# Optimization experiments

Measured on AMD Instinct MI355X. Metric: run time of the kernel, lower is better.

Reference implementation:

```python
import jax, jax.numpy as jnp
import numpy as np

B, T = 64, 512
VOCAB, E, H = 20, 64, 128
D = 2 * H            # 256, bidirectional LSTM output dim
NH, KD = 8, D // 8   # 8 heads, key_dim 32
DU, OUT = 256, 128
NEG = -1e9


def _lstm_scan(x, mask, W, U, b):
    # x: [B,T,E], mask: [B,T] bool. Keras gate order: i, f, g(c), o.
    Bb = x.shape[0]
    Hh = U.shape[0]
    def step(carry, inp):
        h, c = carry
        xt, mt = inp                      # [B,E], [B]
        z = xt @ W + h @ U + b            # [B,4H]
        i, f, g, o = jnp.split(z, 4, axis=-1)
        c_new = jax.nn.sigmoid(f) * c + jax.nn.sigmoid(i) * jnp.tanh(g)
        h_new = jax.nn.sigmoid(o) * jnp.tanh(c_new)
        m = mt[:, None]
        h = jnp.where(m, h_new, h)        # freeze state/output on masked steps
        c = jnp.where(m, c_new, c)
        return (h, c), h
    h0 = jnp.zeros((Bb, Hh), x.dtype)
    _, ys = jax.lax.scan(step, (h0, h0), (jnp.swapaxes(x, 0, 1), mask.T))
    return jnp.swapaxes(ys, 0, 1)         # [B,T,H]


def setup_inputs() -> dict:
    key = jax.random.key(0)
    ks = jax.random.split(key, 24)
    g = lambda k, shape, s: (jax.random.normal(k, shape, jnp.float32) * s)
    inp = {
        'sequences': jax.random.randint(ks[0], (B, T), 0, VOCAB),
        'emb': g(ks[1], (VOCAB, E), 0.05),
        # forward LSTM
        'Wf': g(ks[2], (E, 4 * H), 0.05), 'Uf': g(ks[3], (H, 4 * H), 0.05), 'bf': jnp.zeros((4 * H,), jnp.float32),
        # backward LSTM
        'Wb': g(ks[4], (E, 4 * H), 0.05), 'Ub': g(ks[5], (H, 4 * H), 0.05), 'bb': jnp.zeros((4 * H,), jnp.float32),
        # MHA projections
        'Wq': g(ks[6], (D, NH, KD), 0.05), 'bq': jnp.zeros((NH, KD), jnp.float32),
        'Wk': g(ks[7], (D, NH, KD), 0.05), 'bk': jnp.zeros((NH, KD), jnp.float32),
        'Wv': g(ks[8], (D, NH, KD), 0.05), 'bv': jnp.zeros((NH, KD), jnp.float32),
        'Wo': g(ks[9], (NH, KD, D), 0.05), 'bo': jnp.zeros((D,), jnp.float32),
        # MLP head (input is concat of avg+max pool -> 2*D)
        'W1': g(ks[10], (2 * D, DU), 0.05), 'b1': jnp.zeros((DU,), jnp.float32),
        'W2': g(ks[11], (DU, DU // 2), 0.05), 'b2': jnp.zeros((DU // 2,), jnp.float32),
        'W3': g(ks[12], (DU // 2, OUT), 0.05), 'b3': jnp.zeros((OUT,), jnp.float32),
    }
    return inp


def _forward(sequences, emb, Wf, Uf, bf, Wb, Ub, bb, Wq, bq, Wk, bk, Wv, bv, Wo, bo, W1, b1, W2, b2, W3, b3):
    mask = sequences != 0                       # mask_zero=True
    x = emb[sequences]                          # [B,T,E]
    fwd = _lstm_scan(x, mask, Wf, Uf, bf)
    bwd = _lstm_scan(x[:, ::-1], mask[:, ::-1], Wb, Ub, bb)[:, ::-1]
    h = jnp.concatenate([fwd, bwd], axis=-1)    # [B,T,D]
    # Multi-head self-attention (key-masked, Keras MHA math)
    q = jnp.einsum('btd,dhk->bthk', h, Wq) + bq
    k = jnp.einsum('btd,dhk->bthk', h, Wk) + bk
    v = jnp.einsum('btd,dhk->bthk', h, Wv) + bv
    scores = jnp.einsum('bthk,bshk->bhts', q, k) / jnp.sqrt(jnp.float32(KD))
    scores = jnp.where(mask[:, None, None, :], scores, NEG)
    attn = jax.nn.softmax(scores, axis=-1)      # [B,H,T,T]
    ctx = jnp.einsum('bhts,bshk->bthk', attn, v)
    att = jnp.einsum('bthk,hkd->btd', ctx, Wo) + bo   # [B,T,D]
    # dual pooling (masked mean + masked max)
    mf = mask[..., None].astype(att.dtype)
    avg = (att * mf).sum(axis=1) / jnp.maximum(mf.sum(axis=1), 1.0)
    mx = jnp.where(mask[..., None], att, NEG).max(axis=1)
    p = jnp.concatenate([avg, mx], axis=-1)     # [B,2D]
    x1 = jax.nn.relu(p @ W1 + b1)
    x2 = jax.nn.relu(x1 @ W2 + b2)
    return x2 @ W3 + b3                         # [B,OUT]


def reference(sequences, emb, Wf, Uf, bf, Wb, Ub, bb, Wq, bq, Wk, bk, Wv, bv, Wo, bo, W1, b1, W2, b2, W3, b3):
    return _forward(sequences, emb, Wf, Uf, bf, Wb, Ub, bb, Wq, bq, Wk, bk, Wv, bv, Wo, bo, W1, b1, W2, b2, W3, b3)
```

## Files before the change

### kernel.cpp

```cpp
#include <hip/hip_runtime.h>
#include <math.h>

#define B_ 64
#define T_ 512
#define E_ 64
#define H_ 128
#define NH_ 8
#define KD_ 32
#define BT_ (B_ * T_)
#define NEG_ -1e9f

typedef __attribute__((ext_vector_type(8))) short bf16x8_t;
typedef __attribute__((ext_vector_type(4))) float f32x4_t;
typedef __attribute__((ext_vector_type(2))) float f32x2_t;
typedef unsigned short ushort_t;
typedef unsigned int uint_t;

__device__ __forceinline__ float sigmoidf_(float x) {
    return 1.f / (1.f + __expf(-x));
}
__device__ __forceinline__ float tanhf_(float x) {
    return 1.f - 2.f / (1.f + __expf(2.f * x));
}

__device__ __forceinline__ ushort_t bf16_rne(float x) {
    uint_t u = __float_as_uint(x);
    uint_t r = (u + 0x7FFFu + ((u >> 16) & 1u)) >> 16;
    return (ushort_t)r;
}
__device__ __forceinline__ float bf16_to_f(ushort_t h) {
    return __uint_as_float(((uint_t)h) << 16);
}
__device__ __forceinline__ void split_bf16(float x, ushort_t& h, ushort_t& l) {
    h = bf16_rne(x);
    l = bf16_rne(x - bf16_to_f(h));
}

__device__ __forceinline__ float qswap1(float x) {
    return __int_as_float(__builtin_amdgcn_mov_dpp(__float_as_int(x), 0xB1, 0xF, 0xF, true));
}
__device__ __forceinline__ float qswap2(float x) {
    return __int_as_float(__builtin_amdgcn_mov_dpp(__float_as_int(x), 0x4E, 0xF, 0xF, true));
}

__global__ void prep_kernel(
    const float* __restrict__ emb,
    const float* __restrict__ Wf, const float* __restrict__ bf,
    const float* __restrict__ Wb, const float* __restrict__ bb,
    const float* __restrict__ Wq, const float* __restrict__ Wk,
    const float* __restrict__ Wv, const float* __restrict__ Wo,
    ushort_t* __restrict__ Wqh, ushort_t* __restrict__ Wql,
    ushort_t* __restrict__ Wkh, ushort_t* __restrict__ Wkl,
    ushort_t* __restrict__ Wvh, ushort_t* __restrict__ Wvl,
    ushort_t* __restrict__ Woh, ushort_t* __restrict__ Wol,
    float* __restrict__ embWf, float* __restrict__ embWb)
{
    const int blk = blockIdx.x, tid = threadIdx.x;
    if (blk < 1024) {
        const int m = blk >> 8, k = blk & 255;
        const float* W = (m == 0) ? Wq : (m == 1) ? Wk : (m == 2) ? Wv : Wo;
        ushort_t* Bh = (m == 0) ? Wqh : (m == 1) ? Wkh : (m == 2) ? Wvh : Woh;
        ushort_t* Bl = (m == 0) ? Wql : (m == 1) ? Wkl : (m == 2) ? Wvl : Wol;
        float v = W[k * 256 + tid];
        ushort_t h, l;
        split_bf16(v, h, l);
        Bh[tid * 256 + k] = h;
        Bl[tid * 256 + k] = l;
    } else {
        const int e = blk - 1024;
        const int dir = e >> 1, half = e & 1;
        const float* W = dir ? Wb : Wf;
        const float* bias = dir ? bb : bf;
        float* dst = dir ? embWb : embWf;
        const int np = half * 256 + tid;
        const int gin = ((np & 3) << 7) + (np >> 2);
        for (int v = 0; v < 20; ++v) {
            float acc = bias[gin];
            for (int k = 0; k < 64; ++k)
                acc = fmaf(emb[v * 64 + k], W[k * 512 + gin], acc);
            dst[v * 512 + np] = acc;
        }
    }
}

__global__ __launch_bounds__(256, 2) void gemm_mfma3(
    const ushort_t* __restrict__ Ah, const ushort_t* __restrict__ Al,
    const ushort_t* __restrict__ Bh, const ushort_t* __restrict__ Bl,
    const float* __restrict__ bias, float* __restrict__ C,
    int M, int N)
{
    __shared__ __align__(16) ushort_t Alds[2][128 * 40];
    __shared__ __align__(16) ushort_t Blds[2][128 * 40];

    const int tid = threadIdx.x;
    const int ntn = N >> 7;
    const int bm = blockIdx.x / ntn, bn = blockIdx.x % ntn;
    const int m0 = bm << 7, n0 = bn << 7;

    const int w = tid >> 6;
    const int wr = w >> 1, wc = w & 1;
    const int lane = tid & 63;
    const int fr = lane & 15, kg = lane >> 4;

    const int sr = tid >> 1;
    const int sh = (tid & 1) << 4;

    f32x4_t acc[4][4];
#pragma unroll
    for (int i = 0; i < 4; ++i)
#pragma unroll
        for (int j = 0; j < 4; ++j) acc[i][j] = (f32x4_t){0.f, 0.f, 0.f, 0.f};

    for (int ks = 0; ks < 8; ++ks) {
        const int k0 = ks << 5;
        __syncthreads();
        {
            const size_t ga = (size_t)(m0 + sr) * 256 + k0 + sh;
            const size_t gb = (size_t)(n0 + sr) * 256 + k0 + sh;
            const int ld = sr * 40 + sh;
            const uint4* pah = (const uint4*)(Ah + ga);
            const uint4* pal = (const uint4*)(Al + ga);
            const uint4* pbh = (const uint4*)(Bh + gb);
            const uint4* pbl = (const uint4*)(Bl + gb);
            uint4* qah = (uint4*)&Alds[0][ld];
            uint4* qal = (uint4*)&Alds[1][ld];
            uint4* qbh = (uint4*)&Blds[0][ld];
            uint4* qbl = (uint4*)&Blds[1][ld];
            qah[0] = pah[0]; qah[1] = pah[1];
            qal[0] = pal[0]; qal[1] = pal[1];
            qbh[0] = pbh[0]; qbh[1] = pbh[1];
            qbl[0] = pbl[0]; qbl[1] = pbl[1];
        }
        __syncthreads();

        bf16x8_t ah[4], al[4], bh[4], bl[4];
#pragma unroll
        for (int i = 0; i < 4; ++i) {
            const int ra = (wr * 64 + i * 16 + fr) * 40 + kg * 8;
            const int rb = (wc * 64 + i * 16 + fr) * 40 + kg * 8;
            ah[i] = *(const bf16x8_t*)&Alds[0][ra];
            al[i] = *(const bf16x8_t*)&Alds[1][ra];
            bh[i] = *(const bf16x8_t*)&Blds[0][rb];
            bl[i] = *(const bf16x8_t*)&Blds[1][rb];
        }
#pragma unroll
        for (int i = 0; i < 4; ++i)
#pragma unroll
            for (int j = 0; j < 4; ++j) {
                acc[i][j] = __builtin_amdgcn_mfma_f32_16x16x32_bf16(
                    ah[i], bh[j], acc[i][j], 0, 0, 0);
                acc[i][j] = __builtin_amdgcn_mfma_f32_16x16x32_bf16(
                    ah[i], bl[j], acc[i][j], 0, 0, 0);
                acc[i][j] = __builtin_amdgcn_mfma_f32_16x16x32_bf16(
                    al[i], bh[j], acc[i][j], 0, 0, 0);
            }
    }

#pragma unroll
    for (int j = 0; j < 4; ++j) {
        const int col = n0 + wc * 64 + j * 16 + fr;
        const float bv = bias[col];
#pragma unroll
        for (int i = 0; i < 4; ++i) {
#pragma unroll
            for (int r = 0; r < 4; ++r) {
                const int row = m0 + wr * 64 + i * 16 + kg * 4 + r;
                C[(size_t)row * N + col] = acc[i][j][r] + bv;
            }
        }
    }
}

__global__ __launch_bounds__(512, 1) void lstm_scan(
    const int* __restrict__ seq,
    const float* __restrict__ embWf, const float* __restrict__ embWb,
    const float* __restrict__ Uf, const float* __restrict__ Ub,
    ushort_t* __restrict__ hch, ushort_t* __restrict__ hcl)
{
    const int w = blockIdx.x;
    const int dir = w & 1, b = w >> 1;
    const float* eW = dir ? embWb : embWf;
    const float* U  = dir ? Ub  : Uf;
    const int tid = threadIdx.x;
    const int jj = tid >> 2, ks = tid & 3;

    __shared__ __align__(16) float hbuf[2][4][36];
    __shared__ int tkl[T_];

    f32x2_t u2[4][16];
#pragma unroll
    for (int g = 0; g < 4; ++g)
#pragma unroll
        for (int kk = 0; kk < 16; ++kk) {
            const int kb_ = 32 * ks + 2 * kk;
            u2[g][kk] = (f32x2_t){
                U[(size_t)kb_ * 512 + g * 128 + jj],
                U[(size_t)(kb_ + 1) * 512 + g * 128 + jj] };
        }

    tkl[tid] = seq[b * T_ + tid];
    if (tid < 2 * 4 * 36) ((float*)hbuf)[tid] = 0.f;

    float h_cur = 0.f, c_cur = 0.f;
    ushort_t* hoh = hch + (size_t)b * T_ * 256 + dir * 128;
    ushort_t* hol = hcl + (size_t)b * T_ * 256 + dir * 128;

    __syncthreads();

    int te = dir ? (T_ - 1) : 0;
    int tok = tkl[te];
    float4 xwv = *(const float4*)&eW[tok * 512 + jj * 4];

    int p = 0;
    for (int t = 0; t < T_; ++t) {
        const int te_n  = dir ? (te - 1) : (te + 1);
        const int te_pf = (t == T_ - 1) ? te : te_n;
        const int tok_n = tkl[te_pf];
        const float4 xw_n = *(const float4*)&eW[tok_n * 512 + jj * 4];

        f32x2_t ac0 = {0.f, 0.f}, ac1 = {0.f, 0.f};
        f32x2_t ac2 = {0.f, 0.f}, ac3 = {0.f, 0.f};
        const f32x2_t* hc2 = (const f32x2_t*)hbuf[p][ks];
#pragma unroll
        for (int c = 0; c < 16; ++c) {
            const f32x2_t h2 = hc2[c];
            ac0 = __builtin_elementwise_fma(h2, u2[0][c], ac0);
            ac1 = __builtin_elementwise_fma(h2, u2[1][c], ac1);
            ac2 = __builtin_elementwise_fma(h2, u2[2][c], ac2);
            ac3 = __builtin_elementwise_fma(h2, u2[3][c], ac3);
        }
        float a0 = ac0.x + ac0.y, a1 = ac1.x + ac1.y;
        float a2 = ac2.x + ac2.y, a3 = ac3.x + ac3.y;
        a0 += qswap1(a0); a0 += qswap2(a0);
        a1 += qswap1(a1); a1 += qswap2(a1);
        a2 += qswap1(a2); a2 += qswap2(a2);
        a3 += qswap1(a3); a3 += qswap2(a3);

        const float zi = xwv.x + a0, zf = xwv.y + a1;
        const float zg = xwv.z + a2, zo = xwv.w + a3;
        const float cn = fmaf(sigmoidf_(zf), c_cur, sigmoidf_(zi) * tanhf_(zg));
        const float hn = sigmoidf_(zo) * tanhf_(cn);
        const bool mt = (tok != 0);
        const float hm = mt ? hn : h_cur;
        c_cur = mt ? cn : c_cur;
        h_cur = hm;

        if ((jj >> 5) == ks) hbuf[1 - p][ks][jj & 31] = hm;
        if (ks == 0) {
            ushort_t hh, hl;
            split_bf16(hm, hh, hl);
            hoh[(size_t)te * 256 + jj] = hh;
            hol[(size_t)te * 256 + jj] = hl;
        }
        __syncthreads();
        p ^= 1; te = te_n; tok = tok_n; xwv = xw_n;
    }
}

__global__ __launch_bounds__(256, 2) void attn_fused(
    const int* __restrict__ seq,
    const float* __restrict__ q, const float* __restrict__ kk,
    const float* __restrict__ vv,
    ushort_t* __restrict__ cxh, ushort_t* __restrict__ cxl)
{
    const int wg = blockIdx.x;
    const int b = wg >> 3, h = wg & 7;
    const int tid = threadIdx.x;

    __shared__ __align__(16) float Ks[16][32];
    __shared__ __align__(16) float Vs[16][32];
    __shared__ float mk[16];

    float qA[32], qB[32];
    {
        const float* qp  = q + (((size_t)(b * T_) + tid) * NH_ + h) * KD_;
        const float* qp2 = qp + (size_t)256 * NH_ * KD_;
#pragma unroll
        for (int k = 0; k < 32; k += 4) {
            float4 v0 = *(const float4*)(qp + k);
            float4 v1 = *(const float4*)(qp2 + k);
            qA[k] = v0.x; qA[k + 1] = v0.y; qA[k + 2] = v0.z; qA[k + 3] = v0.w;
            qB[k] = v1.x; qB[k + 1] = v1.y; qB[k + 2] = v1.z; qB[k + 3] = v1.w;
        }
    }
    float ctxA[32], ctxB[32];
#pragma unroll
    for (int k = 0; k < 32; ++k) { ctxA[k] = 0.f; ctxB[k] = 0.f; }
    float mA = -1e30f, mB = -1e30f, lA = 0.f, lB = 0.f;

    const int lr = (tid & 127) >> 3;
    const int lc = (tid & 7) << 2;
    const bool loadV = (tid >= 128);

    for (int c = 0; c < T_ / 16; ++c) {
        const int s0 = c << 4;
        __syncthreads();
        {
            const float* src = (loadV ? vv : kk) +
                (((size_t)(b * T_) + s0 + lr) * NH_ + h) * KD_ + lc;
            float4 v = *(const float4*)src;
            if (loadV) *(float4*)&Vs[lr][lc] = v;
            else       *(float4*)&Ks[lr][lc] = v;
            if (tid < 16) mk[tid] = (seq[b * T_ + s0 + tid] != 0) ? 0.f : 1.f;
        }
        __syncthreads();

        float sA[16], sB[16];
#pragma unroll
        for (int s = 0; s < 16; ++s) {
            float dA = 0.f, dB = 0.f;
#pragma unroll
            for (int k = 0; k < 32; k += 4) {
                float4 k4 = *(const float4*)&Ks[s][k];
                dA = fmaf(k4.x, qA[k], dA); dA = fmaf(k4.y, qA[k + 1], dA);
                dA = fmaf(k4.z, qA[k + 2], dA); dA = fmaf(k4.w, qA[k + 3], dA);
                dB = fmaf(k4.x, qB[k], dB); dB = fmaf(k4.y, qB[k + 1], dB);
                dB = fmaf(k4.z, qB[k + 2], dB); dB = fmaf(k4.w, qB[k + 3], dB);
            }
            const float SCL = 0.17677669529663687f;
            const bool masked = (mk[s] > 0.5f);
            sA[s] = masked ? NEG_ : dA * SCL;
            sB[s] = masked ? NEG_ : dB * SCL;
        }
        float cmA = sA[0], cmB = sB[0];
#pragma unroll
        for (int s = 1; s < 16; ++s) {
            cmA = fmaxf(cmA, sA[s]); cmB = fmaxf(cmB, sB[s]);
        }
        const float mnA = fmaxf(mA, cmA), mnB = fmaxf(mB, cmB);
        const float alA = __expf(mA - mnA), alB = __expf(mB - mnB);
        float psA = 0.f, psB = 0.f;
#pragma unroll
        for (int s = 0; s < 16; ++s) {
            float pa = __expf(sA[s] - mnA); sA[s] = pa; psA += pa;
            float pb = __expf(sB[s] - mnB); sB[s] = pb; psB += pb;
        }
        lA = fmaf(lA, alA, psA); lB = fmaf(lB, alB, psB);
        mA = mnA; mB = mnB;
#pragma unroll
        for (int k = 0; k < 32; ++k) { ctxA[k] *= alA; ctxB[k] *= alB; }
#pragma unroll
        for (int s = 0; s < 16; ++s) {
#pragma unroll
            for (int k = 0; k < 32; k += 4) {
                float4 v4 = *(const float4*)&Vs[s][k];
                ctxA[k]     = fmaf(sA[s], v4.x, ctxA[k]);
                ctxA[k + 1] = fmaf(sA[s], v4.y, ctxA[k + 1]);
                ctxA[k + 2] = fmaf(sA[s], v4.z, ctxA[k + 2]);
                ctxA[k + 3] = fmaf(sA[s], v4.w, ctxA[k + 3]);
                ctxB[k]     = fmaf(sB[s], v4.x, ctxB[k]);
                ctxB[k + 1] = fmaf(sB[s], v4.y, ctxB[k + 1]);
                ctxB[k + 2] = fmaf(sB[s], v4.z, ctxB[k + 2]);
                ctxB[k + 3] = fmaf(sB[s], v4.w, ctxB[k + 3]);
            }
        }
    }

    const float iA = 1.f / lA, iB = 1.f / lB;
    ushort_t* chA = cxh + (((size_t)(b * T_) + tid) * NH_ + h) * KD_;
    ushort_t* clA = cxl + (((size_t)(b * T_) + tid) * NH_ + h) * KD_;
    ushort_t* chB = chA + (size_t)256 * NH_ * KD_;
    ushort_t* clB = clA + (size_t)256 * NH_ * KD_;
#pragma unroll
    for (int k = 0; k < 32; ++k) {
        ushort_t hA, lA_, hB, lB_;
        split_bf16(ctxA[k] * iA, hA, lA_);
        split_bf16(ctxB[k] * iB, hB, lB_);
        chA[k] = hA; clA[k] = lA_;
        chB[k] = hB; clB[k] = lB_;
    }
}

__global__ __launch_bounds__(256) void poolmlp_kernel(
    const int* __restrict__ seq, const float* __restrict__ att,
    const float* __restrict__ W1, const float* __restrict__ b1,
    const float* __restrict__ W2, const float* __restrict__ b2,
    const float* __restrict__ W3, const float* __restrict__ b3,
    float* __restrict__ out)
{
    const int b = blockIdx.x;
    const int tid = threadIdx.x;
    __shared__ float mk[T_];
    __shared__ float pl[512];
    __shared__ float x1l[256];
    __shared__ float x2l[128];

    for (int t = tid; t < T_; t += 256)
        mk[t] = (seq[b * T_ + t] != 0) ? 1.f : 0.f;
    __syncthreads();

    float sum = 0.f, mx = NEG_, cnt = 0.f;
    for (int t = 0; t < T_; ++t) {
        const float a = att[((size_t)b * T_ + t) * 256 + tid];
        const float m = mk[t];
        cnt += m;
        sum = fmaf(m, a, sum);
        mx = fmaxf(mx, (m > 0.5f) ? a : NEG_);
    }
    pl[tid] = sum / fmaxf(cnt, 1.f);
    pl[256 + tid] = mx;
    __syncthreads();

    {
        float acc = b1[tid];
        for (int k = 0; k < 512; ++k) acc = fmaf(pl[k], W1[k * 256 + tid], acc);
        x1l[tid] = fmaxf(acc, 0.f);
    }
    __syncthreads();
    if (tid < 128) {
        float acc = b2[tid];
        for (int k = 0; k < 256; ++k) acc = fmaf(x1l[k], W2[k * 128 + tid], acc);
        x2l[tid] = fmaxf(acc, 0.f);
    }
    __syncthreads();
    if (tid < 128) {
        float acc = b3[tid];
        for (int k = 0; k < 128; ++k) acc = fmaf(x2l[k], W3[k * 128 + tid], acc);
        out[b * 128 + tid] = acc;
    }
}

extern "C" void kernel_launch(void* const* d_in, const int* in_sizes, int n_in,
                              void* d_out, int out_size, void* d_ws, size_t ws_size,
                              hipStream_t stream)
{
    (void)in_sizes; (void)n_in; (void)out_size; (void)ws_size;
    const int*   seq = (const int*)d_in[0];
    const float* emb = (const float*)d_in[1];
    const float* Wf  = (const float*)d_in[2];
    const float* Uf  = (const float*)d_in[3];
    const float* bf  = (const float*)d_in[4];
    const float* Wb  = (const float*)d_in[5];
    const float* Ub  = (const float*)d_in[6];
    const float* bb  = (const float*)d_in[7];
    const float* Wq  = (const float*)d_in[8];
    const float* bq  = (const float*)d_in[9];
    const float* Wk  = (const float*)d_in[10];
    const float* bk  = (const float*)d_in[11];
    const float* Wv  = (const float*)d_in[12];
    const float* bv  = (const float*)d_in[13];
    const float* Wo  = (const float*)d_in[14];
    const float* bo  = (const float*)d_in[15];
    const float* W1  = (const float*)d_in[16];
    const float* b1  = (const float*)d_in[17];
    const float* W2  = (const float*)d_in[18];
    const float* b2  = (const float*)d_in[19];
    const float* W3  = (const float*)d_in[20];
    const float* b3  = (const float*)d_in[21];
    float* out = (float*)d_out;
    float* ws  = (float*)d_ws;

    float* qb   = ws;
    float* kb   = ws + 8388608;
    float* vb   = ws + 16777216;
    ushort_t* cxh = (ushort_t*)(ws + 25165824);
    ushort_t* cxl = cxh + (size_t)BT_ * 256;
    ushort_t* hch = (ushort_t*)(ws + 33554432);
    ushort_t* hcl = hch + (size_t)BT_ * 256;
    float* attb = ws + 33554432;
    ushort_t* wt = (ushort_t*)(ws + 41943040);
    ushort_t* Wqh = wt + 0 * 65536, *Wql = wt + 1 * 65536;
    ushort_t* Wkh = wt + 2 * 65536, *Wkl = wt + 3 * 65536;
    ushort_t* Wvh = wt + 4 * 65536, *Wvl = wt + 5 * 65536;
    ushort_t* Woh = wt + 6 * 65536, *Wol = wt + 7 * 65536;
    float* embWf = ws + 41943040 + 262144;
    float* embWb = embWf + 20 * 512;

    const dim3 blk256(256), blk512(512);

    prep_kernel<<<dim3(1028), blk256, 0, stream>>>(
        emb, Wf, bf, Wb, bb, Wq, Wk, Wv, Wo,
        Wqh, Wql, Wkh, Wkl, Wvh, Wvl, Woh, Wol, embWf, embWb);

    lstm_scan<<<dim3(128), blk512, 0, stream>>>(
        seq, embWf, embWb, Uf, Ub, hch, hcl);

    gemm_mfma3<<<dim3((BT_ / 128) * 2), blk256, 0, stream>>>(
        hch, hcl, Wqh, Wql, bq, qb, BT_, 256);
    gemm_mfma3<<<dim3((BT_ / 128) * 2), blk256, 0, stream>>>(
        hch, hcl, Wkh, Wkl, bk, kb, BT_, 256);
    gemm_mfma3<<<dim3((BT_ / 128) * 2), blk256, 0, stream>>>(
        hch, hcl, Wvh, Wvl, bv, vb, BT_, 256);

    attn_fused<<<dim3(B_ * NH_), blk256, 0, stream>>>(seq, qb, kb, vb, cxh, cxl);

    gemm_mfma3<<<dim3((BT_ / 128) * 2), blk256, 0, stream>>>(
        cxh, cxl, Woh, Wol, bo, attb, BT_, 256);

    poolmlp_kernel<<<dim3(B_), blk256, 0, stream>>>(
        seq, attb, W1, b1, W2, b2, W3, b3, out);
}
```

Before: 945.2 us.

## Fuse QKV projections into one GEMM and slim LSTM scan block

The three Q/K/V projection GEMMs become a single N=768 GEMM with concatenated weights and bias, and attention reads Q, K and V from the interleaved buffer. This removes two launches and re-reads of the hidden-state input. The LSTM scan now uses 256 threads with a 2-way k-split instead of 4-way, so each step needs one DPP reduction instead of two. It keeps the embedding-times-W table in LDS and replaces __syncthreads with a raw waitcnt+barrier. In exchange, each LSTM thread holds twice as many U registers (256 floats), which risks spills and a longer serial FMA chain per step.

Result: slower. 1.057 ms (+11.8%).

```diff
diff --git a/kernel.cpp b/kernel.cpp
--- a/kernel.cpp
+++ b/kernel.cpp
@@ -39,9 +39,6 @@
 __device__ __forceinline__ float qswap1(float x) {
     return __int_as_float(__builtin_amdgcn_mov_dpp(__float_as_int(x), 0xB1, 0xF, 0xF, true));
 }
-__device__ __forceinline__ float qswap2(float x) {
-    return __int_as_float(__builtin_amdgcn_mov_dpp(__float_as_int(x), 0x4E, 0xF, 0xF, true));
-}
 
 __global__ void prep_kernel(
     const float* __restrict__ emb,
@@ -49,24 +46,28 @@
     const float* __restrict__ Wb, const float* __restrict__ bb,
     const float* __restrict__ Wq, const float* __restrict__ Wk,
     const float* __restrict__ Wv, const float* __restrict__ Wo,
-    ushort_t* __restrict__ Wqh, ushort_t* __restrict__ Wql,
-    ushort_t* __restrict__ Wkh, ushort_t* __restrict__ Wkl,
-    ushort_t* __restrict__ Wvh, ushort_t* __restrict__ Wvl,
-    ushort_t* __restrict__ Woh, ushort_t* __restrict__ Wol,
-    float* __restrict__ embWf, float* __restrict__ embWb)
+    const float* __restrict__ bq, const float* __restrict__ bk,
+    const float* __restrict__ bv,
+    ushort_t* __restrict__ wqkvh, ushort_t* __restrict__ wqkvl,
+    ushort_t* __restrict__ woh, ushort_t* __restrict__ wol,
+    float* __restrict__ embWf, float* __restrict__ embWb,
+    float* __restrict__ qkvb)
 {
     const int blk = blockIdx.x, tid = threadIdx.x;
     if (blk < 1024) {
         const int m = blk >> 8, k = blk & 255;
         const float* W = (m == 0) ? Wq : (m == 1) ? Wk : (m == 2) ? Wv : Wo;
-        ushort_t* Bh = (m == 0) ? Wqh : (m == 1) ? Wkh : (m == 2) ? Wvh : Woh;
-        ushort_t* Bl = (m == 0) ? Wql : (m == 1) ? Wkl : (m == 2) ? Wvl : Wol;
         float v = W[k * 256 + tid];
         ushort_t h, l;
         split_bf16(v, h, l);
-        Bh[tid * 256 + k] = h;
-        Bl[tid * 256 + k] = l;
-    } else {
+        if (m < 3) {
+            wqkvh[(m * 256 + tid) * 256 + k] = h;
+            wqkvl[(m * 256 + tid) * 256 + k] = l;
+        } else {
+            woh[tid * 256 + k] = h;
+            wol[tid * 256 + k] = l;
+        }
+    } else if (blk < 1028) {
         const int e = blk - 1024;
         const int dir = e >> 1, half = e & 1;
         const float* W = dir ? Wb : Wf;
@@ -80,6 +81,10 @@
                 acc = fmaf(emb[v * 64 + k], W[k * 512 + gin], acc);
             dst[v * 512 + np] = acc;
         }
+    } else {
+        qkvb[tid] = bq[tid];
+        qkvb[256 + tid] = bk[tid];
+        qkvb[512 + tid] = bv[tid];
     }
 }
 
@@ -171,7 +176,7 @@
     }
 }
 
-__global__ __launch_bounds__(512, 1) void lstm_scan(
+__global__ __launch_bounds__(256, 1) void lstm_scan(
     const int* __restrict__ seq,
     const float* __restrict__ embWf, const float* __restrict__ embWb,
     const float* __restrict__ Uf, const float* __restrict__ Ub,
@@ -182,24 +187,31 @@
     const float* eW = dir ? embWb : embWf;
     const float* U  = dir ? Ub  : Uf;
     const int tid = threadIdx.x;
-    const int jj = tid >> 2, ks = tid & 3;
-
-    __shared__ __align__(16) float hbuf[2][4][36];
+    const int jj = tid >> 1, ks = tid & 1;
+
+    __shared__ __align__(16) float eWl[20 * 512];
+    __shared__ __align__(16) float hbuf[2][136];
     __shared__ int tkl[T_];
 
-    f32x2_t u2[4][16];
+    f32x2_t u2[4][32];
 #pragma unroll
     for (int g = 0; g < 4; ++g)
 #pragma unroll
-        for (int kk = 0; kk < 16; ++kk) {
-            const int kb_ = 32 * ks + 2 * kk;
-            u2[g][kk] = (f32x2_t){
+        for (int c = 0; c < 32; ++c) {
+            const int kb_ = 64 * ks + 2 * c;
+            u2[g][c] = (f32x2_t){
                 U[(size_t)kb_ * 512 + g * 128 + jj],
                 U[(size_t)(kb_ + 1) * 512 + g * 128 + jj] };
         }
 
-    tkl[tid] = seq[b * T_ + tid];
-    if (tid < 2 * 4 * 36) ((float*)hbuf)[tid] = 0.f;
+    {
+        const float4* src = (const float4*)eW;
+        float4* dst = (float4*)eWl;
+        for (int i = tid; i < 2560; i += 256) dst[i] = src[i];
+        tkl[tid] = seq[b * T_ + tid];
+        tkl[tid + 256] = seq[b * T_ + 256 + tid];
+        for (int i = tid; i < 272; i += 256) ((float*)hbuf)[i] = 0.f;
+    }
 
     float h_cur = 0.f, c_cur = 0.f;
     ushort_t* hoh = hch + (size_t)b * T_ * 256 + dir * 128;
@@ -209,20 +221,20 @@
 
     int te = dir ? (T_ - 1) : 0;
     int tok = tkl[te];
-    float4 xwv = *(const float4*)&eW[tok * 512 + jj * 4];
+    float4 xwv = *(const float4*)&eWl[tok * 512 + jj * 4];
 
     int p = 0;
     for (int t = 0; t < T_; ++t) {
         const int te_n  = dir ? (te - 1) : (te + 1);
         const int te_pf = (t == T_ - 1) ? te : te_n;
         const int tok_n = tkl[te_pf];
-        const float4 xw_n = *(const float4*)&eW[tok_n * 512 + jj * 4];
+        const float4 xw_n = *(const float4*)&eWl[tok_n * 512 + jj * 4];
 
         f32x2_t ac0 = {0.f, 0.f}, ac1 = {0.f, 0.f};
         f32x2_t ac2 = {0.f, 0.f}, ac3 = {0.f, 0.f};
-        const f32x2_t* hc2 = (const f32x2_t*)hbuf[p][ks];
-#pragma unroll
-        for (int c = 0; c < 16; ++c) {
+        const f32x2_t* hc2 = (const f32x2_t*)&hbuf[p][68 * ks];
+#pragma unroll
+        for (int c = 0; c < 32; ++c) {
             const f32x2_t h2 = hc2[c];
             ac0 = __builtin_elementwise_fma(h2, u2[0][c], ac0);
             ac1 = __builtin_elementwise_fma(h2, u2[1][c], ac1);
@@ -231,10 +243,10 @@
         }
         float a0 = ac0.x + ac0.y, a1 = ac1.x + ac1.y;
         float a2 = ac2.x + ac2.y, a3 = ac3.x + ac3.y;
-        a0 += qswap1(a0); a0 += qswap2(a0);
-        a1 += qswap1(a1); a1 += qswap2(a1);
-        a2 += qswap1(a2); a2 += qswap2(a2);
-        a3 += qswap1(a3); a3 += qswap2(a3);
+        a0 += qswap1(a0);
+        a1 += qswap1(a1);
+        a2 += qswap1(a2);
+        a3 += qswap1(a3);
 
         const float zi = xwv.x + a0, zf = xwv.y + a1;
         const float zg = xwv.z + a2, zo = xwv.w + a3;
@@ -245,22 +257,22 @@
         c_cur = mt ? cn : c_cur;
         h_cur = hm;
 
-        if ((jj >> 5) == ks) hbuf[1 - p][ks][jj & 31] = hm;
         if (ks == 0) {
+            const int pos = (jj < 64) ? jj : jj + 4;
+            hbuf[1 - p][pos] = hm;
             ushort_t hh, hl;
             split_bf16(hm, hh, hl);
             hoh[(size_t)te * 256 + jj] = hh;
             hol[(size_t)te * 256 + jj] = hl;
         }
-        __syncthreads();
+        asm volatile("s_waitcnt lgkmcnt(0)\n\ts_barrier" ::: "memory");
         p ^= 1; te = te_n; tok = tok_n; xwv = xw_n;
     }
 }
 
 __global__ __launch_bounds__(256, 2) void attn_fused(
     const int* __restrict__ seq,
-    const float* __restrict__ q, const float* __restrict__ kk,
-    const float* __restrict__ vv,
+    const float* __restrict__ qkv,
     ushort_t* __restrict__ cxh, ushort_t* __restrict__ cxl)
 {
     const int wg = blockIdx.x;
@@ -273,8 +285,8 @@
 
     float qA[32], qB[32];
     {
-        const float* qp  = q + (((size_t)(b * T_) + tid) * NH_ + h) * KD_;
-        const float* qp2 = qp + (size_t)256 * NH_ * KD_;
+        const float* qp  = qkv + ((size_t)(b * T_) + tid) * 768 + h * KD_;
+        const float* qp2 = qp + (size_t)256 * 768;
 #pragma unroll
         for (int k = 0; k < 32; k += 4) {
             float4 v0 = *(const float4*)(qp + k);
@@ -296,8 +308,8 @@
         const int s0 = c << 4;
         __syncthreads();
         {
-            const float* src = (loadV ? vv : kk) +
-                (((size_t)(b * T_) + s0 + lr) * NH_ + h) * KD_ + lc;
+            const float* src = qkv + ((size_t)(b * T_) + s0 + lr) * 768 +
+                               (loadV ? 512 : 256) + h * KD_ + lc;
             float4 v = *(const float4*)src;
             if (loadV) *(float4*)&Vs[lr][lc] = v;
             else       *(float4*)&Ks[lr][lc] = v;
@@ -450,42 +462,37 @@
     float* out = (float*)d_out;
     float* ws  = (float*)d_ws;
 
-    float* qb   = ws;
-    float* kb   = ws + 8388608;
-    float* vb   = ws + 16777216;
+    float* qkv  = ws;
     ushort_t* cxh = (ushort_t*)(ws + 25165824);
     ushort_t* cxl = cxh + (size_t)BT_ * 256;
     ushort_t* hch = (ushort_t*)(ws + 33554432);
     ushort_t* hcl = hch + (size_t)BT_ * 256;
     float* attb = ws + 33554432;
     ushort_t* wt = (ushort_t*)(ws + 41943040);
-    ushort_t* Wqh = wt + 0 * 65536, *Wql = wt + 1 * 65536;
-    ushort_t* Wkh = wt + 2 * 65536, *Wkl = wt + 3 * 65536;
-    ushort_t* Wvh = wt + 4 * 65536, *Wvl = wt + 5 * 65536;
-    ushort_t* Woh = wt + 6 * 65536, *Wol = wt + 7 * 65536;
+    ushort_t* wqkvh = wt;
+    ushort_t* wqkvl = wt + 196608;
+    ushort_t* woh   = wt + 393216;
+    ushort_t* wol   = wt + 458752;
     float* embWf = ws + 41943040 + 262144;
     float* embWb = embWf + 20 * 512;
-
-    const dim3 blk256(256), blk512(512);
-
-    prep_kernel<<<dim3(1028), blk256, 0, stream>>>(
-        emb, Wf, bf, Wb, bb, Wq, Wk, Wv, Wo,
-        Wqh, Wql, Wkh, Wkl, Wvh, Wvl, Woh, Wol, embWf, embWb);
-
-    lstm_scan<<<dim3(128), blk512, 0, stream>>>(
+    float* qkvb  = embWb + 20 * 512;
+
+    const dim3 blk256(256);
+
+    prep_kernel<<<dim3(1029), blk256, 0, stream>>>(
+        emb, Wf, bf, Wb, bb, Wq, Wk, Wv, Wo, bq, bk, bv,
+        wqkvh, wqkvl, woh, wol, embWf, embWb, qkvb);
+
+    lstm_scan<<<dim3(128), blk256, 0, stream>>>(
         seq, embWf, embWb, Uf, Ub, hch, hcl);
 
+    gemm_mfma3<<<dim3((BT_ / 128) * 6), blk256, 0, stream>>>(
+        hch, hcl, wqkvh, wqkvl, qkvb, qkv, BT_, 768);
+
+    attn_fused<<<dim3(B_ * NH_), blk256, 0, stream>>>(seq, qkv, cxh, cxl);
+
     gemm_mfma3<<<dim3((BT_ / 128) * 2), blk256, 0, stream>>>(
-        hch, hcl, Wqh, Wql, bq, qb, BT_, 256);
-    gemm_mfma3<<<dim3((BT_ / 128) * 2), blk256, 0, stream>>>(
-        hch, hcl, Wkh, Wkl, bk, kb, BT_, 256);
-    gemm_mfma3<<<dim3((BT_ / 128) * 2), blk256, 0, stream>>>(
-        hch, hcl, Wvh, Wvl, bv, vb, BT_, 256);
-
-    attn_fused<<<dim3(B_ * NH_), blk256, 0, stream>>>(seq, qb, kb, vb, cxh, cxl);
-
-    gemm_mfma3<<<dim3((BT_ / 128) * 2), blk256, 0, stream>>>(
-        cxh, cxl, Woh, Wol, bo, attb, BT_, 256);
+        cxh, cxl, woh, wol, bo, attb, BT_, 256);
 
     poolmlp_kernel<<<dim3(B_), blk256, 0, stream>>>(
         seq, attb, W1, b1, W2, b2, W3, b3, out);
```
